# Optimization experiments

Measured on AMD Instinct MI355X. Metric: run time of the kernel, lower is better.

The kernel has to match this reference:

```python
import jax, jax.numpy as jnp
import numpy as np

N_ACT = 100000   # number of candidate actions (batch)
ATOM = 64        # atom_max + 1 (action slot + neighbors, padded)
N_SPEC = 3       # len(elements) + 1 ('action' pseudo-species)
N_EMB = 10
N_FIT = 32
N_SUB = N_EMB // 4  # 2


def setup_inputs() -> dict:
    key = jax.random.key(0)
    ks = jax.random.split(key, 24)
    inp = {
        "Smat": jax.random.uniform(ks[0], (N_ACT, ATOM), dtype=jnp.float32),
        "Rraw": jax.random.normal(ks[1], (N_ACT, ATOM, 4), dtype=jnp.float32),
        "mask_species": jax.random.uniform(ks[2], (N_ACT, ATOM, N_SPEC), dtype=jnp.float32),
    }
    def lin(kw, kb, fan_in, fan_out):
        s = 1.0 / np.sqrt(fan_in)
        W = jax.random.uniform(kw, (fan_in, fan_out), minval=-s, maxval=s, dtype=jnp.float32)
        b = jax.random.uniform(kb, (fan_out,), minval=-s, maxval=s, dtype=jnp.float32)
        return W, b
    inp["W_e1"], inp["b_e1"] = lin(ks[3], ks[4], N_SPEC, N_EMB)
    inp["W_e2"], inp["b_e2"] = lin(ks[5], ks[6], N_EMB, N_EMB)
    D_IN = N_SUB * N_EMB  # 20
    inp["W_f1"], inp["b_f1"] = lin(ks[7], ks[8], D_IN, N_FIT)
    inp["W_f2"], inp["b_f2"] = lin(ks[9], ks[10], N_FIT, N_FIT)
    inp["W_f3"], inp["b_f3"] = lin(ks[11], ks[12], N_FIT, 1)
    inp["W_v1"], inp["b_v1"] = lin(ks[13], ks[14], D_IN, N_FIT)
    inp["W_v2"], inp["b_v2"] = lin(ks[15], ks[16], N_FIT, N_FIT)
    inp["W_v3"], inp["b_v3"] = lin(ks[17], ks[18], N_FIT, 1)
    return inp


def _contract(G, R):
    # einsum('ijk,ijl,iml,imn->ikn', G[:,:,:N_SUB], R, R, G) done as two small GEMMs
    A = jnp.einsum('ijk,ijl->ikl', G[..., :N_SUB], R)   # [n, N_SUB, 4]
    B = jnp.einsum('iml,imn->iln', R, G)                # [n, 4, N_EMB]
    return jnp.einsum('ikl,iln->ikn', A, B)             # [n, N_SUB, N_EMB]


def _mlp3(x, W1, b1, W2, b2, W3, b3):
    h = jax.nn.relu(x @ W1 + b1)
    h = jax.nn.relu(h @ W2 + b2)
    return h @ W3 + b3


def reference(Smat, Rraw, mask_species,
              W_e1, b_e1, W_e2, b_e2,
              W_f1, b_f1, W_f2, b_f2, W_f3, b_f3,
              W_v1, b_v1, W_v2, b_v2, W_v3, b_v3):
    R = Smat[..., None] * Rraw                          # [n, ATOM, 4]
    Sg = Smat[..., None] * mask_species                 # [n, ATOM, N_SPEC]
    G = jax.nn.relu(Sg @ W_e1 + b_e1) @ W_e2 + b_e2     # [n, ATOM, N_EMB]

    D = _contract(G, R).reshape(Smat.shape[0], N_SUB * N_EMB)
    policy = jax.nn.log_softmax(_mlp3(D, W_f1, b_f1, W_f2, b_f2, W_f3, b_f3).ravel())

    Dval = _contract(G[:, 1:], R[:, 1:]).reshape(Smat.shape[0], N_SUB * N_EMB)
    value = jnp.sum(_mlp3(Dval, W_v1, b_v1, W_v2, b_v2, W_v3, b_v3).ravel())
    return policy, value
```

## Files before the change

kernel.cpp:

```cpp
#include <hip/hip_runtime.h>
#include <math.h>

#define ATOM 64


__device__ __forceinline__ float full_head(const float (&x)[20],
                                           const float* __restrict__ w1, const float* __restrict__ b1,
                                           const float* __restrict__ w2, const float* __restrict__ b2,
                                           const float* __restrict__ w3)
{
    float h1[32];
#pragma unroll
    for (int q=0;q<8;++q) {
        float4 b = *(const float4*)(b1 + 4*q);
        h1[4*q+0]=b.x; h1[4*q+1]=b.y; h1[4*q+2]=b.z; h1[4*q+3]=b.w;
    }
#pragma unroll
    for (int d=0; d<20; ++d) {
        const float xv = x[d];
        const float* row = w1 + d*32;
#pragma unroll
        for (int q=0;q<8;++q) {
            float4 w = *(const float4*)(row + 4*q);
            h1[4*q+0] += xv*w.x; h1[4*q+1] += xv*w.y;
            h1[4*q+2] += xv*w.z; h1[4*q+3] += xv*w.w;
        }
    }
    float p[32];
#pragma unroll
    for (int q=0;q<8;++q) {
        float4 b = *(const float4*)(b2 + 4*q);
        p[4*q+0]=b.x; p[4*q+1]=b.y; p[4*q+2]=b.z; p[4*q+3]=b.w;
    }
#pragma unroll
    for (int o=0;o<32;++o) {
        const float hv = fmaxf(h1[o], 0.f);
        const float* row = w2 + o*32;
#pragma unroll
        for (int q=0;q<8;++q) {
            float4 w = *(const float4*)(row + 4*q);
            p[4*q+0] += hv*w.x; p[4*q+1] += hv*w.y;
            p[4*q+2] += hv*w.z; p[4*q+3] += hv*w.w;
        }
    }
    float s = 0.f;
#pragma unroll
    for (int q=0;q<8;++q) {
        float4 wq = *(const float4*)(w3 + 4*q);
        s += fmaxf(p[4*q+0], 0.f)*wq.x;
        s += fmaxf(p[4*q+1], 0.f)*wq.y;
        s += fmaxf(p[4*q+2], 0.f)*wq.z;
        s += fmaxf(p[4*q+3], 0.f)*wq.w;
    }
    return s;
}

__global__ __launch_bounds__(256) void k_embed(
    const float* __restrict__ Smat, const float* __restrict__ Rraw, const float* __restrict__ Mspec,
    const float* __restrict__ We1, const float* __restrict__ be1,
    float* __restrict__ Vws, float* __restrict__ A0ws, int n)
{
    const int tid = threadIdx.x;
    const int j   = tid & 3;
    const int grp = tid >> 2;
    const int act = blockIdx.x*64 + grp;
    const bool active = act < n;
    const int actc = active ? act : (n-1);

    float e1w0[10], e1w1[10], e1w2[10], e1w3[10];
#pragma unroll
    for (int e=0;e<10;++e){
        e1w0[e]=be1[e]; e1w1[e]=We1[e]; e1w2[e]=We1[10+e]; e1w3[e]=We1[20+e];
    }

    const float4* rp = (const float4*)Rraw + (size_t)actc*ATOM + j;
    const float*  sp = Smat  + (size_t)actc*ATOM + j;
    const float*  mp = Mspec + (size_t)actc*(ATOM*3) + 3*j;

    float Bh[4][10];
    float Rsum[4] = {0.f,0.f,0.f,0.f};
#pragma unroll
    for (int l=0;l<4;++l)
#pragma unroll
        for (int e=0;e<10;++e) Bh[l][e]=0.f;

    float a0h[10], a0r[4];
#pragma unroll
    for (int e=0;e<10;++e) a0h[e]=0.f;
    a0r[0]=a0r[1]=a0r[2]=a0r[3]=0.f;

    float4 rN  = rp[0];
    float  sN  = sp[0];
    float  m0N = mp[0], m1N = mp[1], m2N = mp[2];

#pragma unroll 1
    for (int u=0; u<16; ++u) {
        const float4 r  = rN;
        const float  s  = sN;
        const float  m0 = m0N, m1 = m1N, m2 = m2N;
        if (u < 15) {
            rN  = rp[4*(u+1)];
            sN  = sp[4*(u+1)];
            m0N = mp[12*(u+1)]; m1N = mp[12*(u+1)+1]; m2N = mp[12*(u+1)+2];
        }
        const float Rl0=s*r.x, Rl1=s*r.y, Rl2=s*r.z, Rl3=s*r.w;
        const float sg0=s*m0, sg1=s*m1, sg2=s*m2;
        float h[10];
#pragma unroll
        for (int e=0;e<10;++e)
            h[e] = fmaxf(0.f, e1w0[e] + sg0*e1w1[e] + sg1*e1w2[e] + sg2*e1w3[e]);
        Rsum[0]+=Rl0; Rsum[1]+=Rl1; Rsum[2]+=Rl2; Rsum[3]+=Rl3;
#pragma unroll
        for (int e=0;e<10;++e){
            const float he=h[e];
            Bh[0][e]+=Rl0*he; Bh[1][e]+=Rl1*he; Bh[2][e]+=Rl2*he; Bh[3][e]+=Rl3*he;
        }
        if (u==0 && j==0){
#pragma unroll
            for (int e=0;e<10;++e) a0h[e]=h[e];
            a0r[0]=Rl0; a0r[1]=Rl1; a0r[2]=Rl2; a0r[3]=Rl3;
        }
    }

#pragma unroll
    for (int l=0;l<4;++l) {
        float v=Rsum[l]; v+=__shfl_xor(v,1); v+=__shfl_xor(v,2); Rsum[l]=v;
#pragma unroll
        for (int e=0;e<10;++e) {
            float w=Bh[l][e]; w+=__shfl_xor(w,1); w+=__shfl_xor(w,2); Bh[l][e]=w;
        }
    }

    if (!active) return;
    const size_t N = (size_t)n;
    if (j==0) {
#pragma unroll
        for (int e=0;e<10;++e) Vws[(size_t)e*N + act] = Bh[0][e];
        Vws[(size_t)40*N + act] = Rsum[0];
#pragma unroll
        for (int e=0;e<10;++e) A0ws[(size_t)e*N + act] = a0h[e];
#pragma unroll
        for (int l=0;l<4;++l)  A0ws[(size_t)(10+l)*N + act] = a0r[l];
    } else if (j==1) {
#pragma unroll
        for (int e=0;e<10;++e) Vws[(size_t)(10+e)*N + act] = Bh[1][e];
        Vws[(size_t)41*N + act] = Rsum[1];
    } else if (j==2) {
#pragma unroll
        for (int e=0;e<10;++e) Vws[(size_t)(20+e)*N + act] = Bh[2][e];
        Vws[(size_t)42*N + act] = Rsum[2];
    } else {
#pragma unroll
        for (int e=0;e<10;++e) Vws[(size_t)(30+e)*N + act] = Bh[3][e];
        Vws[(size_t)43*N + act] = Rsum[3];
    }
}

__global__ __launch_bounds__(256) void k_head(
    const float* __restrict__ Vws, const float* __restrict__ A0ws,
    const float* __restrict__ We2, const float* __restrict__ be2,
    const float* __restrict__ Wf1, const float* __restrict__ bf1,
    const float* __restrict__ Wf2, const float* __restrict__ bf2,
    const float* __restrict__ Wf3, const float* __restrict__ bf3,
    const float* __restrict__ Wv1, const float* __restrict__ bv1,
    const float* __restrict__ Wv2, const float* __restrict__ bv2,
    const float* __restrict__ Wv3, const float* __restrict__ bv3,
    float* __restrict__ logits, float* __restrict__ pmax,
    float* __restrict__ psum, float* __restrict__ pval, int n)
{
    __shared__ __align__(16) float s_e2[10][12];
    __shared__ __align__(16) float s_f1[640], s_v1[640];
    __shared__ __align__(16) float s_f2[1024], s_v2[1024];
    __shared__ __align__(16) float s_b1[32], s_b2[32], s_f3[32];
    __shared__ __align__(16) float s_bv1[32], s_bv2[32], s_v3[32];
    __shared__ float red_l[128], red_v[128];

    const int tid = threadIdx.x;
    for (int i=tid;i<640;i+=256){ s_f1[i]=Wf1[i]; s_v1[i]=Wv1[i]; }
    for (int i=tid;i<1024;i+=256){ s_f2[i]=Wf2[i]; s_v2[i]=Wv2[i]; }
    if (tid<32){ s_b1[tid]=bf1[tid]; s_b2[tid]=bf2[tid]; s_f3[tid]=Wf3[tid];
                 s_bv1[tid]=bv1[tid]; s_bv2[tid]=bv2[tid]; s_v3[tid]=Wv3[tid]; }
    if (tid<10){
        s_e2[tid][0] = be2[tid];
        for (int e=0;e<10;++e) s_e2[tid][1+e] = We2[e*10+tid];
        s_e2[tid][11] = 0.f;
    }
    __syncthreads();

    const int half = tid >> 7;
    const int idx  = tid & 127;
    const int act  = blockIdx.x*128 + idx;
    const bool active = act < n;
    const int actc = active ? act : (n-1);
    const size_t N = (size_t)n;

    float Bh[4][10], Rsum[4];
#pragma unroll
    for (int l=0;l<4;++l)
#pragma unroll
        for (int e=0;e<10;++e) Bh[l][e] = Vws[(size_t)(l*10+e)*N + actc];
#pragma unroll
    for (int l=0;l<4;++l) Rsum[l] = Vws[(size_t)(40+l)*N + actc];

    if (half) {
        float h0[10], r0[4];
#pragma unroll
        for (int e=0;e<10;++e) h0[e] = A0ws[(size_t)e*N + actc];
#pragma unroll
        for (int l=0;l<4;++l)  r0[l] = A0ws[(size_t)(10+l)*N + actc];
#pragma unroll
        for (int l=0;l<4;++l){
            Rsum[l] -= r0[l];
#pragma unroll
            for (int e=0;e<10;++e) Bh[l][e] -= r0[l]*h0[e];
        }
    }

    float Bk0[4], Bk1[4];
#pragma unroll
    for (int k=0;k<2;++k){
        const float4 c0 = *(const float4*)&s_e2[k][0];
        const float4 c1 = *(const float4*)&s_e2[k][4];
        const float4 c2 = *(const float4*)&s_e2[k][8];
#pragma unroll
        for (int l=0;l<4;++l){
            const float v = Rsum[l]*c0.x + Bh[l][0]*c0.y + Bh[l][1]*c0.z + Bh[l][2]*c0.w
                          + Bh[l][3]*c1.x + Bh[l][4]*c1.y + Bh[l][5]*c1.z + Bh[l][6]*c1.w
                          + Bh[l][7]*c2.x + Bh[l][8]*c2.y + Bh[l][9]*c2.z;
            if (k==0) Bk0[l]=v; else Bk1[l]=v;
        }
    }
    float D[20];
#pragma unroll
    for (int q=0;q<10;++q){
        const float4 c0 = *(const float4*)&s_e2[q][0];
        const float4 c1 = *(const float4*)&s_e2[q][4];
        const float4 c2 = *(const float4*)&s_e2[q][8];
        float Bq[4];
#pragma unroll
        for (int l=0;l<4;++l)
            Bq[l] = Rsum[l]*c0.x + Bh[l][0]*c0.y + Bh[l][1]*c0.z + Bh[l][2]*c0.w
                  + Bh[l][3]*c1.x + Bh[l][4]*c1.y + Bh[l][5]*c1.z + Bh[l][6]*c1.w
                  + Bh[l][7]*c2.x + Bh[l][8]*c2.y + Bh[l][9]*c2.z;
        D[q]    = Bk0[0]*Bq[0]+Bk0[1]*Bq[1]+Bk0[2]*Bq[2]+Bk0[3]*Bq[3];
        D[10+q] = Bk1[0]*Bq[0]+Bk1[1]*Bq[1]+Bk1[2]*Bq[2]+Bk1[3]*Bq[3];
    }

    const float* w1 = half ? s_v1  : s_f1;
    const float* b1 = half ? s_bv1 : s_b1;
    const float* w2 = half ? s_v2  : s_f2;
    const float* b2 = half ? s_bv2 : s_b2;
    const float* w3 = half ? s_v3  : s_f3;
    const float  b3 = half ? bv3[0] : bf3[0];
    const float  out = full_head(D, w1, b1, w2, b2, w3) + b3;

    if (half == 0) {
        red_l[idx] = active ? out : -INFINITY;
        if (active) logits[act] = out;
    } else {
        red_v[idx] = active ? out : 0.f;
    }
    __syncthreads();

    if (tid < 64) {
        float m = fmaxf(red_l[tid], red_l[tid+64]);
#pragma unroll
        for (int k=1;k<64;k<<=1) m = fmaxf(m, __shfl_xor(m,k));
        float ssum = expf(red_l[tid]-m) + expf(red_l[tid+64]-m);
        float vsum = red_v[tid] + red_v[tid+64];
#pragma unroll
        for (int k=1;k<64;k<<=1){ ssum += __shfl_xor(ssum,k); vsum += __shfl_xor(vsum,k); }
        if (tid==0){ pmax[blockIdx.x]=m; psum[blockIdx.x]=ssum; pval[blockIdx.x]=vsum; }
    }
}

__device__ __forceinline__ void make_D(const float (&Bh)[4][10], const float (&Rsum)[4],
                                       const float (*e2)[12], float (&D)[20])
{
    float Bk[2][4];
#pragma unroll
    for (int k=0;k<2;++k) {
        const float4 c0 = *(const float4*)&e2[k][0];
        const float4 c1 = *(const float4*)&e2[k][4];
        const float4 c2 = *(const float4*)&e2[k][8];
#pragma unroll
        for (int l=0;l<4;++l) {
            Bk[k][l] = Rsum[l]*c0.x + Bh[l][0]*c0.y + Bh[l][1]*c0.z + Bh[l][2]*c0.w
                     + Bh[l][3]*c1.x + Bh[l][4]*c1.y + Bh[l][5]*c1.z + Bh[l][6]*c1.w
                     + Bh[l][7]*c2.x + Bh[l][8]*c2.y + Bh[l][9]*c2.z;
        }
    }
#pragma unroll
    for (int q=0;q<10;++q) {
        const float4 c0 = *(const float4*)&e2[q][0];
        const float4 c1 = *(const float4*)&e2[q][4];
        const float4 c2 = *(const float4*)&e2[q][8];
        float Bq[4];
#pragma unroll
        for (int l=0;l<4;++l) {
            Bq[l] = Rsum[l]*c0.x + Bh[l][0]*c0.y + Bh[l][1]*c0.z + Bh[l][2]*c0.w
                  + Bh[l][3]*c1.x + Bh[l][4]*c1.y + Bh[l][5]*c1.z + Bh[l][6]*c1.w
                  + Bh[l][7]*c2.x + Bh[l][8]*c2.y + Bh[l][9]*c2.z;
        }
        D[q]    = Bk[0][0]*Bq[0]+Bk[0][1]*Bq[1]+Bk[0][2]*Bq[2]+Bk[0][3]*Bq[3];
        D[10+q] = Bk[1][0]*Bq[0]+Bk[1][1]*Bq[1]+Bk[1][2]*Bq[2]+Bk[1][3]*Bq[3];
    }
}

__device__ __forceinline__ float mlp_head_quad(const float* __restrict__ x,
                                          const float* __restrict__ w1, const float* __restrict__ b1,
                                          const float* __restrict__ w2, const float* __restrict__ b2,
                                          const float* __restrict__ w3, int j)
{
    float h1[8];
    {
        float4 ba = *(const float4*)(b1 + 8*j);
        float4 bb = *(const float4*)(b1 + 8*j + 4);
        h1[0]=ba.x; h1[1]=ba.y; h1[2]=ba.z; h1[3]=ba.w;
        h1[4]=bb.x; h1[5]=bb.y; h1[6]=bb.z; h1[7]=bb.w;
    }
#pragma unroll
    for (int d=0; d<20; ++d) {
        float4 w0 = *(const float4*)(w1 + d*32 + 8*j);
        float4 w4 = *(const float4*)(w1 + d*32 + 8*j + 4);
        float xv = x[d];
        h1[0] += xv*w0.x; h1[1] += xv*w0.y; h1[2] += xv*w0.z; h1[3] += xv*w0.w;
        h1[4] += xv*w4.x; h1[5] += xv*w4.y; h1[6] += xv*w4.z; h1[7] += xv*w4.w;
    }
#pragma unroll
    for (int o=0;o<8;++o) h1[o] = fmaxf(h1[o], 0.f);

    float s = 0.f;
#pragma unroll
    for (int half=0; half<2; ++half) {
        float p[16];
#pragma unroll
        for (int q=0;q<16;++q) p[q] = 0.f;
#pragma unroll
        for (int o=0;o<8;++o) {
            const float* row = w2 + (8*j + o)*32 + 16*half;
            float hv = h1[o];
#pragma unroll
            for (int q=0;q<4;++q) {
                float4 w = *(const float4*)(row + 4*q);
                p[4*q+0] += hv*w.x; p[4*q+1] += hv*w.y;
                p[4*q+2] += hv*w.z; p[4*q+3] += hv*w.w;
            }
        }
#pragma unroll
        for (int q=0;q<16;++q) { p[q] += __shfl_xor(p[q],1); p[q] += __shfl_xor(p[q],2); }
#pragma unroll
        for (int q=0;q<4;++q) {
            float4 bq = *(const float4*)(b2 + 16*half + 4*q);
            float4 wq = *(const float4*)(w3 + 16*half + 4*q);
            s += fmaxf(p[4*q+0]+bq.x, 0.f)*wq.x;
            s += fmaxf(p[4*q+1]+bq.y, 0.f)*wq.y;
            s += fmaxf(p[4*q+2]+bq.z, 0.f)*wq.z;
            s += fmaxf(p[4*q+3]+bq.w, 0.f)*wq.w;
        }
    }
    return s;
}

__global__ __launch_bounds__(256) void k_fused(
    const float* __restrict__ Smat, const float* __restrict__ Rraw, const float* __restrict__ Mspec,
    const float* __restrict__ We1, const float* __restrict__ be1,
    const float* __restrict__ We2, const float* __restrict__ be2,
    const float* __restrict__ Wf1, const float* __restrict__ bf1,
    const float* __restrict__ Wf2, const float* __restrict__ bf2,
    const float* __restrict__ Wf3, const float* __restrict__ bf3,
    const float* __restrict__ Wv1, const float* __restrict__ bv1,
    const float* __restrict__ Wv2, const float* __restrict__ bv2,
    const float* __restrict__ Wv3, const float* __restrict__ bv3,
    float* __restrict__ logits, float* __restrict__ pmax,
    float* __restrict__ psum, float* __restrict__ pval, int n)
{
    __shared__ __align__(16) float4 s_e1[10];
    __shared__ __align__(16) float  s_e2[10][12];
    __shared__ __align__(16) float  s_f1[640], s_v1[640];
    __shared__ __align__(16) float  s_f2[1024], s_v2[1024];
    __shared__ __align__(16) float  s_b1[32], s_b2[32], s_f3[32];
    __shared__ __align__(16) float  s_bv1[32], s_bv2[32], s_v3[32];
    __shared__ __align__(16) float  s_a0[64][16];
    __shared__ float red_l[64], red_v[64];

    const int tid = threadIdx.x;
    for (int i=tid;i<640;i+=256){ s_f1[i]=Wf1[i]; s_v1[i]=Wv1[i]; }
    for (int i=tid;i<1024;i+=256){ s_f2[i]=Wf2[i]; s_v2[i]=Wv2[i]; }
    if (tid<32){ s_b1[tid]=bf1[tid]; s_b2[tid]=bf2[tid]; s_f3[tid]=Wf3[tid];
                 s_bv1[tid]=bv1[tid]; s_bv2[tid]=bv2[tid]; s_v3[tid]=Wv3[tid]; }
    if (tid<10){
        s_e1[tid] = make_float4(be1[tid], We1[tid], We1[10+tid], We1[20+tid]);
        s_e2[tid][0] = be2[tid];
        for (int e=0;e<10;++e) s_e2[tid][1+e] = We2[e*10+tid];
        s_e2[tid][11] = 0.f;
    }
    __syncthreads();

    const int j    = tid & 3;
    const int grp  = tid >> 2;
    const int act  = blockIdx.x*64 + grp;
    const bool active = act < n;
    const int actc = active ? act : (n-1);

    const float*  sp = Smat + (size_t)actc*ATOM;
    const float4* rp = (const float4*)Rraw  + (size_t)actc*ATOM;
    const float4* mp = (const float4*)Mspec + (size_t)actc*48;

    float Bh[4][10];
    float Rsum[4] = {0.f,0.f,0.f,0.f};
#pragma unroll
    for (int l=0;l<4;++l)
#pragma unroll
        for (int e=0;e<10;++e) Bh[l][e]=0.f;

#pragma unroll 1
    for (int c=0;c<4;++c) {
        const int a0 = 16*j + 4*c;
        const float4 s4 = *(const float4*)(sp + a0);
        const float4 rv0 = rp[a0+0];
        const float4 rv1 = rp[a0+1];
        const float4 rv2 = rp[a0+2];
        const float4 rv3 = rp[a0+3];
        const float4 mA = mp[12*j+3*c+0];
        const float4 mB = mp[12*j+3*c+1];
        const float4 mC = mp[12*j+3*c+2];

        const float  sv[4]  = {s4.x,s4.y,s4.z,s4.w};
        const float4 rv[4]  = {rv0,rv1,rv2,rv3};
        const float  mk[12] = {mA.x,mA.y,mA.z,mA.w,mB.x,mB.y,mB.z,mB.w,mC.x,mC.y,mC.z,mC.w};

#pragma unroll
        for (int u=0;u<4;++u) {
            const float s   = sv[u];
            const float Rl0 = s*rv[u].x, Rl1 = s*rv[u].y, Rl2 = s*rv[u].z, Rl3 = s*rv[u].w;
            const float sg0 = s*mk[3*u+0], sg1 = s*mk[3*u+1], sg2 = s*mk[3*u+2];
            float h[10];
#pragma unroll
            for (int e=0;e<10;++e) {
                const float4 w = s_e1[e];
                h[e] = fmaxf(0.f, w.x + sg0*w.y + sg1*w.z + sg2*w.w);
            }
            Rsum[0]+=Rl0; Rsum[1]+=Rl1; Rsum[2]+=Rl2; Rsum[3]+=Rl3;
#pragma unroll
            for (int e=0;e<10;++e) {
                const float he = h[e];
                Bh[0][e]+=Rl0*he; Bh[1][e]+=Rl1*he; Bh[2][e]+=Rl2*he; Bh[3][e]+=Rl3*he;
            }
            if (c==0 && u==0 && j==0) {
#pragma unroll
                for (int e=0;e<10;++e) s_a0[grp][e]=h[e];
                s_a0[grp][10]=Rl0; s_a0[grp][11]=Rl1; s_a0[grp][12]=Rl2; s_a0[grp][13]=Rl3;
            }
        }
    }

#pragma unroll
    for (int l=0;l<4;++l) {
        float v=Rsum[l]; v+=__shfl_xor(v,1); v+=__shfl_xor(v,2); Rsum[l]=v;
#pragma unroll
        for (int e=0;e<10;++e) {
            float w=Bh[l][e]; w+=__shfl_xor(w,1); w+=__shfl_xor(w,2); Bh[l][e]=w;
        }
    }

    float Df[20];
    make_D(Bh, Rsum, s_e2, Df);
    {
        const float* a0p = &s_a0[grp][0];
#pragma unroll
        for (int l=0;l<4;++l) {
            const float r0 = a0p[10+l];
            Rsum[l] -= r0;
#pragma unroll
            for (int e=0;e<10;++e) Bh[l][e] -= r0*a0p[e];
        }
    }
    float Dv[20];
    make_D(Bh, Rsum, s_e2, Dv);

    const float logit = mlp_head_quad(Df, s_f1, s_b1, s_f2, s_b2, s_f3, j) + bf3[0];
    const float vout  = mlp_head_quad(Dv, s_v1, s_bv1, s_v2, s_bv2, s_v3, j) + bv3[0];

    if (j==0) {
        red_l[grp] = active ? logit : -INFINITY;
        red_v[grp] = active ? vout  : 0.f;
        if (active) logits[act] = logit;
    }
    __syncthreads();

    if (tid < 64) {
        float m = red_l[tid];
#pragma unroll
        for (int k=1;k<64;k<<=1) m = fmaxf(m, __shfl_xor(m,k));
        float e = expf(red_l[tid] - m);
        float ssum = e, vsum = red_v[tid];
#pragma unroll
        for (int k=1;k<64;k<<=1){ ssum += __shfl_xor(ssum,k); vsum += __shfl_xor(vsum,k); }
        if (tid==0){ pmax[blockIdx.x]=m; psum[blockIdx.x]=ssum; pval[blockIdx.x]=vsum; }
    }
}

__global__ __launch_bounds__(256) void k_reduce(const float* __restrict__ pmax,
                                                const float* __restrict__ psum,
                                                const float* __restrict__ pval,
                                                int nb,
                                                float* __restrict__ logZ,
                                                float* __restrict__ value_out)
{
    __shared__ float sm[256];
    const int tid = threadIdx.x;
    float m = -INFINITY;
    for (int i=tid;i<nb;i+=256) m = fmaxf(m, pmax[i]);
    sm[tid]=m; __syncthreads();
    for (int s=128;s>0;s>>=1){ if (tid<s) sm[tid]=fmaxf(sm[tid],sm[tid+s]); __syncthreads(); }
    const float M = sm[0]; __syncthreads();

    float ssum=0.f, vsum=0.f;
    for (int i=tid;i<nb;i+=256){ ssum += psum[i]*expf(pmax[i]-M); vsum += pval[i]; }
    sm[tid]=ssum; __syncthreads();
    for (int s=128;s>0;s>>=1){ if (tid<s) sm[tid]+=sm[tid+s]; __syncthreads(); }
    const float S = sm[0]; __syncthreads();

    sm[tid]=vsum; __syncthreads();
    for (int s=128;s>0;s>>=1){ if (tid<s) sm[tid]+=sm[tid+s]; __syncthreads(); }
    if (tid==0){ *logZ = M + logf(S); *value_out = sm[0]; }
}

__global__ __launch_bounds__(256) void k_apply(const float* __restrict__ logits,
                                               const float* __restrict__ logZ,
                                               float* __restrict__ out, int n)
{
    const int i = blockIdx.x*256 + threadIdx.x;
    if (i < n) out[i] = logits[i] - logZ[0];
}

extern "C" void kernel_launch(void* const* d_in, const int* in_sizes, int n_in,
                              void* d_out, int out_size, void* d_ws, size_t ws_size,
                              hipStream_t stream)
{
    const float* Smat  = (const float*)d_in[0];
    const float* Rraw  = (const float*)d_in[1];
    const float* Mspec = (const float*)d_in[2];
    const float* We1 = (const float*)d_in[3];  const float* be1 = (const float*)d_in[4];
    const float* We2 = (const float*)d_in[5];  const float* be2 = (const float*)d_in[6];
    const float* Wf1 = (const float*)d_in[7];  const float* bf1 = (const float*)d_in[8];
    const float* Wf2 = (const float*)d_in[9];  const float* bf2 = (const float*)d_in[10];
    const float* Wf3 = (const float*)d_in[11]; const float* bf3 = (const float*)d_in[12];
    const float* Wv1 = (const float*)d_in[13]; const float* bv1 = (const float*)d_in[14];
    const float* Wv2 = (const float*)d_in[15]; const float* bv2 = (const float*)d_in[16];
    const float* Wv3 = (const float*)d_in[17]; const float* bv3 = (const float*)d_in[18];

    const int n   = in_sizes[0] / ATOM;
    const int nbE = (n + 63) / 64;
    const int nbH = (n + 127) / 128;

    float* out = (float*)d_out;
    const size_t need_new = ((size_t)58*n + (size_t)n + 3*(size_t)nbH + 16) * sizeof(float);

    if (ws_size >= need_new) {
        float* ws     = (float*)d_ws;
        float* Vws    = ws;
        float* A0ws   = Vws + (size_t)44*n;
        float* logits = A0ws + (size_t)14*n;
        float* pmax   = logits + n;
        float* psum   = pmax + nbH;
        float* pval   = psum + nbH;
        float* logZ   = pval + nbH;

        k_embed<<<nbE, 256, 0, stream>>>(Smat, Rraw, Mspec, We1, be1, Vws, A0ws, n);
        k_head<<<nbH, 256, 0, stream>>>(Vws, A0ws, We2, be2,
                                        Wf1, bf1, Wf2, bf2, Wf3, bf3,
                                        Wv1, bv1, Wv2, bv2, Wv3, bv3,
                                        logits, pmax, psum, pval, n);
        k_reduce<<<1, 256, 0, stream>>>(pmax, psum, pval, nbH, logZ, out + n);
        k_apply<<<(n + 255)/256, 256, 0, stream>>>(logits, logZ, out, n);
    } else {
        float* ws     = (float*)d_ws;
        float* logits = ws;
        float* pmax   = ws + n;
        float* psum   = pmax + nbE;
        float* pval   = psum + nbE;
        float* logZ   = pval + nbE;

        k_fused<<<nbE, 256, 0, stream>>>(Smat, Rraw, Mspec,
                                         We1, be1, We2, be2,
                                         Wf1, bf1, Wf2, bf2, Wf3, bf3,
                                         Wv1, bv1, Wv2, bv2, Wv3, bv3,
                                         logits, pmax, psum, pval, n);
        k_reduce<<<1, 256, 0, stream>>>(pmax, psum, pval, nbE, logZ, out + n);
        k_apply<<<(n + 255)/256, 256, 0, stream>>>(logits, logZ, out, n);
    }
}
```

Measured before the change: 93.90 us.

## Stage embed-kernel inputs through LDS with double-buffered global_load_lds

The embed kernel now loads each action's rows of Rraw, Mspec and Smat with direct global-to-LDS loads, 8 atoms per chunk, into double-buffered shared memory. Each lane of a wave loads one action's row, so the global reads are contiguous per row and can be prefetched one chunk ahead. Threads then read their atoms from LDS in a transposed, padded layout. This replaces strided per-thread register prefetches with overlapped async copies, at the cost of hand-written vmcnt waits and two barriers per chunk, which is fragile if the count of outstanding loads does not match.

```diff
diff --git a/kernel.cpp b/kernel.cpp
--- a/kernel.cpp
+++ b/kernel.cpp
@@ -2,7 +2,15 @@
 #include <math.h>
 
 #define ATOM 64
-
+#define AS1 __attribute__((address_space(1)))
+#define AS3 __attribute__((address_space(3)))
+
+__device__ __forceinline__ void gl16(const void* g, void* l) {
+    __builtin_amdgcn_global_load_lds((const AS1 void*)g, (AS3 void*)l, 16, 0, 0);
+}
+__device__ __forceinline__ void gl4(const void* g, void* l) {
+    __builtin_amdgcn_global_load_lds((const AS1 void*)g, (AS3 void*)l, 4, 0, 0);
+}
 
 __device__ __forceinline__ float full_head(const float (&x)[20],
                                            const float* __restrict__ w1, const float* __restrict__ b1,
@@ -60,12 +68,18 @@
     const float* __restrict__ We1, const float* __restrict__ be1,
     float* __restrict__ Vws, float* __restrict__ A0ws, int n)
 {
-    const int tid = threadIdx.x;
-    const int j   = tid & 3;
-    const int grp = tid >> 2;
-    const int act = blockIdx.x*64 + grp;
+    __shared__ __align__(16) float4 lds_R[2][8*66];
+    __shared__ __align__(16) float  lds_M[2][24*68];
+    __shared__ __align__(16) float  lds_S[2][8*68];
+
+    const int tid  = threadIdx.x;
+    const int w    = tid >> 6;
+    const int lane = tid & 63;
+    const int j    = tid & 3;
+    const int grp  = tid >> 2;
+    const int act0 = blockIdx.x*64;
+    const int act  = act0 + grp;
     const bool active = act < n;
-    const int actc = active ? act : (n-1);
 
     float e1w0[10], e1w1[10], e1w2[10], e1w3[10];
 #pragma unroll
@@ -73,9 +87,10 @@
         e1w0[e]=be1[e]; e1w1[e]=We1[e]; e1w2[e]=We1[10+e]; e1w3[e]=We1[20+e];
     }
 
-    const float4* rp = (const float4*)Rraw + (size_t)actc*ATOM + j;
-    const float*  sp = Smat  + (size_t)actc*ATOM + j;
-    const float*  mp = Mspec + (size_t)actc*(ATOM*3) + 3*j;
+    const int arow = min(act0 + lane, n-1);
+    const char* gRb = (const char*)Rraw  + (size_t)arow*1024;
+    const char* gSb = (const char*)Smat  + (size_t)arow*256;
+    const char* gMb = (const char*)Mspec + (size_t)arow*768;
 
     float Bh[4][10];
     float Rsum[4] = {0.f,0.f,0.f,0.f};
@@ -89,37 +104,68 @@
     for (int e=0;e<10;++e) a0h[e]=0.f;
     a0r[0]=a0r[1]=a0r[2]=a0r[3]=0.f;
 
-    float4 rN  = rp[0];
-    float  sN  = sp[0];
-    float  m0N = mp[0], m1N = mp[1], m2N = mp[2];
-
+    auto issue = [&](int c, int b){
+        const char* r = gRb + c*128;
+        const char* m = gMb + c*96;
+        const char* s = gSb + c*32;
 #pragma unroll 1
-    for (int u=0; u<16; ++u) {
-        const float4 r  = rN;
-        const float  s  = sN;
-        const float  m0 = m0N, m1 = m1N, m2 = m2N;
-        if (u < 15) {
-            rN  = rp[4*(u+1)];
-            sN  = sp[4*(u+1)];
-            m0N = mp[12*(u+1)]; m1N = mp[12*(u+1)+1]; m2N = mp[12*(u+1)+2];
-        }
-        const float Rl0=s*r.x, Rl1=s*r.y, Rl2=s*r.z, Rl3=s*r.w;
-        const float sg0=s*m0, sg1=s*m1, sg2=s*m2;
-        float h[10];
-#pragma unroll
-        for (int e=0;e<10;++e)
-            h[e] = fmaxf(0.f, e1w0[e] + sg0*e1w1[e] + sg1*e1w2[e] + sg2*e1w3[e]);
-        Rsum[0]+=Rl0; Rsum[1]+=Rl1; Rsum[2]+=Rl2; Rsum[3]+=Rl3;
-#pragma unroll
-        for (int e=0;e<10;++e){
-            const float he=h[e];
-            Bh[0][e]+=Rl0*he; Bh[1][e]+=Rl1*he; Bh[2][e]+=Rl2*he; Bh[3][e]+=Rl3*he;
-        }
-        if (u==0 && j==0){
-#pragma unroll
-            for (int e=0;e<10;++e) a0h[e]=h[e];
-            a0r[0]=Rl0; a0r[1]=Rl1; a0r[2]=Rl2; a0r[3]=Rl3;
-        }
+        for (int it = w; it < 40; it += 4) {
+            if (it < 8) {
+                gl16(r + it*16, &lds_R[b][it*66]);
+            } else if (it < 32) {
+                gl4(m + (it-8)*4, &lds_M[b][(it-8)*68]);
+            } else {
+                gl4(s + (it-32)*4, &lds_S[b][(it-32)*68]);
+            }
+        }
+    };
+
+    auto compute = [&](int b, bool first){
+#pragma unroll
+        for (int u=0; u<2; ++u){
+            const int t = 4*u + j;
+            const float4 r = lds_R[b][t*66 + grp];
+            const float  s = lds_S[b][t*68 + grp];
+            const float  m0 = lds_M[b][(3*t+0)*68 + grp];
+            const float  m1 = lds_M[b][(3*t+1)*68 + grp];
+            const float  m2 = lds_M[b][(3*t+2)*68 + grp];
+
+            const float Rl0=s*r.x, Rl1=s*r.y, Rl2=s*r.z, Rl3=s*r.w;
+            const float sg0=s*m0, sg1=s*m1, sg2=s*m2;
+            float h[10];
+#pragma unroll
+            for (int e=0;e<10;++e)
+                h[e] = fmaxf(0.f, e1w0[e] + sg0*e1w1[e] + sg1*e1w2[e] + sg2*e1w3[e]);
+            Rsum[0]+=Rl0; Rsum[1]+=Rl1; Rsum[2]+=Rl2; Rsum[3]+=Rl3;
+#pragma unroll
+            for (int e=0;e<10;++e){
+                const float he=h[e];
+                Bh[0][e]+=Rl0*he; Bh[1][e]+=Rl1*he; Bh[2][e]+=Rl2*he; Bh[3][e]+=Rl3*he;
+            }
+            if (first && u==0 && j==0){
+#pragma unroll
+                for (int e=0;e<10;++e) a0h[e]=h[e];
+                a0r[0]=Rl0; a0r[1]=Rl1; a0r[2]=Rl2; a0r[3]=Rl3;
+            }
+        }
+    };
+
+    issue(0, 0);
+    asm volatile("s_waitcnt vmcnt(0)" ::: "memory");
+    __builtin_amdgcn_s_barrier();
+
+#pragma unroll 1
+    for (int c=0; c<8; ++c){
+        if (c < 7) {
+            issue(c+1, (c+1)&1);
+            asm volatile("s_waitcnt vmcnt(10)" ::: "memory");
+        } else {
+            asm volatile("s_waitcnt vmcnt(0)" ::: "memory");
+        }
+        __builtin_amdgcn_s_barrier();
+        compute(c&1, c==0);
+        asm volatile("s_waitcnt lgkmcnt(0)" ::: "memory");
+        __builtin_amdgcn_s_barrier();
     }
 
 #pragma unroll
@@ -127,7 +173,7 @@
         float v=Rsum[l]; v+=__shfl_xor(v,1); v+=__shfl_xor(v,2); Rsum[l]=v;
 #pragma unroll
         for (int e=0;e<10;++e) {
-            float w=Bh[l][e]; w+=__shfl_xor(w,1); w+=__shfl_xor(w,2); Bh[l][e]=w;
+            float ww=Bh[l][e]; ww+=__shfl_xor(ww,1); ww+=__shfl_xor(ww,2); Bh[l][e]=ww;
         }
     }
 
```

Result: slower. 125.1 us (+33.3%).
